# Kernel optimization log

Hardware: AMD Instinct MI355X
Metric: run time of the kernel (lower is better)

## Reference

```python
import jax, jax.numpy as jnp
import numpy as np

D_MODEL = 1024
D_FF = 4096
N_EXPERTS = 8
TOP_K = 2

def setup_inputs() -> dict:
    key = jax.random.key(0)
    ks = jax.random.split(key, 8)
    s = 1.0 / np.sqrt(D_MODEL)
    sf = 1.0 / np.sqrt(D_FF)
    return {
        "x": jax.random.normal(ks[0], (4, 1024, D_MODEL), dtype=jnp.float32),
        "W1": jax.random.uniform(ks[1], (N_EXPERTS, D_MODEL, D_FF), jnp.float32, -s, s),
        "b1": jax.random.uniform(ks[2], (N_EXPERTS, D_FF), jnp.float32, -s, s),
        "W2": jax.random.uniform(ks[3], (N_EXPERTS, D_FF, D_MODEL), jnp.float32, -sf, sf),
        "b2": jax.random.uniform(ks[4], (N_EXPERTS, D_MODEL), jnp.float32, -sf, sf),
        "Wg": jax.random.uniform(ks[5], (D_MODEL, N_EXPERTS), jnp.float32, -s, s),
        "bg": jax.random.uniform(ks[6], (N_EXPERTS,), jnp.float32, -s, s),
    }

def reference(x, W1, b1, W2, b2, Wg, bg):
    # gate: [B,S,E]
    logits = jnp.einsum('bsd,de->bse', x, Wg) + bg
    probs = jax.nn.softmax(logits, axis=-1)
    # top-k mask + renormalize (k < n_experts)
    topk_vals, topk_idx = jax.lax.top_k(probs, TOP_K)
    mask = jax.nn.one_hot(topk_idx, N_EXPERTS, dtype=probs.dtype).sum(axis=-2)
    probs = probs * mask
    denom = probs.sum(axis=-1, keepdims=True)
    denom = denom + (denom == 0).astype(probs.dtype)
    probs = probs / denom
    # dense expert compute: all experts on all tokens. h: [B,E,S,d_ff]
    h = jnp.einsum('bsd,edf->besf', x, W1) + b1[None, :, None, :]
    h = jax.nn.gelu(h, approximate=False)
    y = jnp.einsum('besf,efd->besd', h, W2) + b2[None, :, None, :]
    # weighted combine over experts: [B,S,d]
    out = jnp.einsum('bse,besd->bsd', probs, y)
    return out
```

## Files before the change

### kernel.cpp

```cpp
#include <hip/hip_runtime.h>
#include <hip/hip_bf16.h>

#define NTOK   4096
#define DMODEL 1024
#define DFF    4096
#define NEXP   8
#define TOPK   2
#define BM 128
#define BN 128
#define BK 64
#define NSLOT   (NTOK*TOPK)
#define MAXSLOT (NSLOT + NEXP*BM)
#define MAXTILE (MAXSLOT/BM)

typedef __attribute__((ext_vector_type(8))) short bf16x8;
typedef __attribute__((ext_vector_type(8))) unsigned short u16x8;
typedef __attribute__((ext_vector_type(4))) float f32x4;

__device__ __forceinline__ unsigned short f2bf(float f){
    union { float f; unsigned int u; } v; v.f = f;
    unsigned int r = (v.u + 0x7fffu + ((v.u >> 16) & 1u)) >> 16;
    return (unsigned short)r;
}

__device__ __forceinline__ void gload16(const unsigned short* g, unsigned short* l){
    __builtin_amdgcn_global_load_lds(
        (const __attribute__((address_space(1))) void*)g,
        (__attribute__((address_space(3))) void*)l,
        16, 0, 0);
}

__global__ __launch_bounds__(256) void k_transpose_convert(const float* __restrict__ src,
                                                           unsigned short* __restrict__ dst,
                                                           int R, int C)
{
    __shared__ unsigned short tile[64][72];
    src += (size_t)blockIdx.z * R * C;
    dst += (size_t)blockIdx.z * R * C;
    int r0 = blockIdx.y * 64, c0 = blockIdx.x * 64;
    int t = threadIdx.x;
    int tr = t >> 4;
    int tc = (t & 15) * 4;
    #pragma unroll
    for(int i=0;i<4;i++){
        float4 v = *(const float4*)&src[(size_t)(r0 + tr + i*16)*C + c0 + tc];
        tile[tc+0][tr + i*16] = f2bf(v.x);
        tile[tc+1][tr + i*16] = f2bf(v.y);
        tile[tc+2][tr + i*16] = f2bf(v.z);
        tile[tc+3][tr + i*16] = f2bf(v.w);
    }
    __syncthreads();
    int rr  = t >> 3;
    int cc8 = (t & 7) * 8;
    #pragma unroll
    for(int i=0;i<2;i++){
        u16x8 o = *(const u16x8*)&tile[rr + i*32][cc8];
        *(u16x8*)&dst[(size_t)(c0 + rr + i*32)*R + r0 + cc8] = o;
    }
}

__global__ __launch_bounds__(256) void k_gate(const float* __restrict__ x,
                                              const float* __restrict__ Wg,
                                              const float* __restrict__ bg,
                                              unsigned short* __restrict__ Xb,
                                              int* __restrict__ token_e,
                                              float* __restrict__ token_w,
                                              int* __restrict__ cnt)
{
    int tid = threadIdx.x;
    const float4* xs = (const float4*)x + (size_t)blockIdx.x * 1024;
    ushort4* xd = (ushort4*)Xb + (size_t)blockIdx.x * 1024;
    #pragma unroll
    for(int rep=0;rep<4;rep++){
        float4 v = xs[rep*256 + tid];
        ushort4 o; o.x=f2bf(v.x); o.y=f2bf(v.y); o.z=f2bf(v.z); o.w=f2bf(v.w);
        xd[rep*256 + tid] = o;
    }

    int wid = tid >> 6, lane = tid & 63;
    int t = blockIdx.x * 4 + wid;
    const float* xr = x + (size_t)t * DMODEL;
    float pe[NEXP];
    #pragma unroll
    for(int e=0;e<NEXP;e++) pe[e] = 0.f;
    for(int i=0;i<DMODEL/64;i++){
        int d = i*64 + lane;
        float xv = xr[d];
        const float* wr = Wg + (size_t)d * NEXP;
        #pragma unroll
        for(int e=0;e<NEXP;e++) pe[e] += xv * wr[e];
    }
    #pragma unroll
    for(int off=32; off>0; off>>=1){
        #pragma unroll
        for(int e=0;e<NEXP;e++) pe[e] += __shfl_xor(pe[e], off);
    }
    if(lane == 0){
        float lg[NEXP], mx = -1e30f;
        #pragma unroll
        for(int e=0;e<NEXP;e++){ lg[e] = pe[e] + bg[e]; mx = fmaxf(mx, lg[e]); }
        float pr[NEXP];
        #pragma unroll
        for(int e=0;e<NEXP;e++) pr[e] = expf(lg[e] - mx);
        int e0 = 0; float p0 = pr[0];
        #pragma unroll
        for(int e=1;e<NEXP;e++) if(pr[e] > p0){ p0 = pr[e]; e0 = e; }
        int e1 = -1; float p1 = -1.f;
        #pragma unroll
        for(int e=0;e<NEXP;e++) if(e != e0 && pr[e] > p1){ p1 = pr[e]; e1 = e; }
        float dn = p0 + p1;
        token_e[2*t]   = e0; token_w[2*t]   = p0/dn;
        token_e[2*t+1] = e1; token_w[2*t+1] = p1/dn;
        atomicAdd(&cnt[e0], 1); atomicAdd(&cnt[e1], 1);
    }
}

__global__ __launch_bounds__(256) void k_prefix_scatter(const int* __restrict__ cnt,
                                                        const int* __restrict__ token_e,
                                                        const float* __restrict__ token_w,
                                                        int* __restrict__ tile_e,
                                                        int* __restrict__ tile_row0,
                                                        int* __restrict__ tile_valid,
                                                        int* __restrict__ slot_token,
                                                        float* __restrict__ slot_w)
{
    __shared__ int sb[NEXP], scur[NEXP];
    int tid = threadIdx.x;
    if(tid == 0){
        int off = 0, nt = 0;
        for(int e=0;e<NEXP;e++){
            sb[e] = off; scur[e] = 0;
            int c = cnt[e];
            for(int r=0;r<c;r+=BM){
                tile_e[nt] = e; tile_row0[nt] = off + r;
                tile_valid[nt] = (c - r < BM) ? (c - r) : BM;
                nt++;
            }
            off += ((c + BM - 1)/BM)*BM;
        }
        for(int i=nt;i<MAXTILE;i++){ tile_e[i]=0; tile_row0[i]=0; tile_valid[i]=0; }
    }
    for(int s=tid; s<MAXSLOT; s+=256) slot_token[s] = 0;
    __syncthreads();
    for(int i=tid; i<NSLOT; i+=256){
        int e = token_e[i];
        int s = sb[e] + atomicAdd(&scur[e], 1);
        slot_token[s] = i >> 1;
        slot_w[s] = token_w[i];
    }
}

template<bool GATHER, bool GELU>
__global__ __launch_bounds__(256) void k_gemm(const unsigned short* __restrict__ A,
                                              const unsigned short* __restrict__ Bw,
                                              const float* __restrict__ bias,
                                              const int* __restrict__ tile_e,
                                              const int* __restrict__ tile_row0,
                                              const int* __restrict__ tile_valid,
                                              const int* __restrict__ slot_token,
                                              const float* __restrict__ slot_w,
                                              unsigned short* __restrict__ OutH,
                                              float* __restrict__ outF,
                                              int K, int N)
{
    int tid = blockIdx.x;
    int valid = tile_valid[tid];
    if(valid == 0) return;
    int e = tile_e[tid];
    int row0 = tile_row0[tid];
    int n0 = blockIdx.y * BN;
    const unsigned short* Be = Bw + (size_t)e * N * K;

    __shared__ unsigned short As[BM*BK];
    __shared__ unsigned short Bs[BN*BK];

    int t = threadIdx.x;
    int lane = t & 63;
    int wid = t >> 6;
    int wr = wid >> 1, wc = wid & 1;

    int srow = t >> 3;
    int csw  = (t & 7) ^ (srow & 7);
    const unsigned short* arow[4];
    const unsigned short* brow[4];
    #pragma unroll
    for(int i=0;i<4;i++){
        int r = i*32 + srow;
        size_t aoff;
        if(GATHER) aoff = (size_t)slot_token[row0 + r] * (size_t)K;
        else       aoff = (size_t)(row0 + r) * (size_t)K;
        arow[i] = A  + aoff + csw*8;
        brow[i] = Be + (size_t)(n0 + r)*K + csw*8;
    }
    unsigned short* alds = As + (size_t)t * 8;
    unsigned short* blds = Bs + (size_t)t * 8;

    f32x4 acc[4][4];
    #pragma unroll
    for(int m=0;m<4;m++)
        #pragma unroll
        for(int n=0;n<4;n++)
            acc[m][n] = (f32x4){0.f,0.f,0.f,0.f};

    int rl = lane & 15;
    int g  = lane >> 4;
    int rx = rl & 7;

    for(int k0=0;k0<K;k0+=BK){
        __syncthreads();
        #pragma unroll
        for(int i=0;i<4;i++){
            gload16(arow[i] + k0, alds + i*2048);
            gload16(brow[i] + k0, blds + i*2048);
        }
        __syncthreads();

        #pragma unroll
        for(int kb=0;kb<2;kb++){
            int sw = ((kb*4 + g) ^ rx) * 8;
            bf16x8 af[4], bfv[4];
            #pragma unroll
            for(int m=0;m<4;m++) af[m]  = *(const bf16x8*)&As[(wr*64 + m*16 + rl)*BK + sw];
            #pragma unroll
            for(int n=0;n<4;n++) bfv[n] = *(const bf16x8*)&Bs[(wc*64 + n*16 + rl)*BK + sw];
            #pragma unroll
            for(int m=0;m<4;m++)
                #pragma unroll
                for(int n=0;n<4;n++)
                    acc[m][n] = __builtin_amdgcn_mfma_f32_16x16x32_bf16(af[m], bfv[n], acc[m][n], 0, 0, 0);
        }
    }

    const float* be = bias + (size_t)e * N;
    #pragma unroll
    for(int m=0;m<4;m++){
        int rb = wr*64 + m*16 + ((lane>>4)<<2);
        #pragma unroll
        for(int j=0;j<4;j++){
            int r = rb + j;
            if(r >= valid) continue;
            size_t grow = (size_t)(row0 + r);
            if(GELU){
                #pragma unroll
                for(int n=0;n<4;n++){
                    int col = n0 + wc*64 + n*16 + rl;
                    float v = acc[m][n][j] + be[col];
                    v = 0.5f * v * (1.f + erff(v * 0.70710678118654752f));
                    OutH[grow * (size_t)N + col] = f2bf(v);
                }
            } else {
                float wsc = slot_w[grow];
                float* orow = outF + (size_t)slot_token[grow] * DMODEL;
                #pragma unroll
                for(int n=0;n<4;n++){
                    int col = n0 + wc*64 + n*16 + rl;
                    float v = (acc[m][n][j] + be[col]) * wsc;
                    atomicAdd(&orow[col], v);
                }
            }
        }
    }
}

extern "C" void kernel_launch(void* const* d_in, const int* in_sizes, int n_in,
                              void* d_out, int out_size, void* d_ws, size_t ws_size,
                              hipStream_t stream)
{
    const float* x  = (const float*)d_in[0];
    const float* W1 = (const float*)d_in[1];
    const float* b1 = (const float*)d_in[2];
    const float* W2 = (const float*)d_in[3];
    const float* b2 = (const float*)d_in[4];
    const float* Wg = (const float*)d_in[5];
    const float* bg = (const float*)d_in[6];
    float* out = (float*)d_out;

    char* p = (char*)d_ws;
    auto alloc = [&](size_t bytes)->char*{
        char* r = p; p += (bytes + 255) & ~(size_t)255; return r;
    };
    unsigned short* W1t = (unsigned short*)alloc((size_t)NEXP*DFF*DMODEL*2);
    unsigned short* W2t = (unsigned short*)alloc((size_t)NEXP*DMODEL*DFF*2);
    unsigned short* Xb  = (unsigned short*)alloc((size_t)NTOK*DMODEL*2);
    unsigned short* H   = (unsigned short*)alloc((size_t)MAXSLOT*DFF*2);
    int*   slot_token = (int*)alloc(MAXSLOT*4);
    float* slot_w     = (float*)alloc(MAXSLOT*4);
    int*   token_e    = (int*)alloc(NSLOT*4);
    float* token_w    = (float*)alloc(NSLOT*4);
    int*   cnt        = (int*)alloc(32);
    int*   tile_e     = (int*)alloc(MAXTILE*4);
    int*   tile_row0  = (int*)alloc(MAXTILE*4);
    int*   tile_valid = (int*)alloc(MAXTILE*4);
    (void)ws_size; (void)in_sizes; (void)n_in; (void)out_size;

    hipMemsetAsync(cnt, 0, 32, stream);
    hipMemsetAsync(out, 0, (size_t)NTOK*DMODEL*4, stream);
    k_gate<<<NTOK/4, 256, 0, stream>>>(x, Wg, bg, Xb, token_e, token_w, cnt);
    k_transpose_convert<<<dim3(DFF/64, DMODEL/64, NEXP), 256, 0, stream>>>(W1, W1t, DMODEL, DFF);
    k_transpose_convert<<<dim3(DMODEL/64, DFF/64, NEXP), 256, 0, stream>>>(W2, W2t, DFF, DMODEL);
    k_prefix_scatter<<<1, 256, 0, stream>>>(cnt, token_e, token_w,
                                            tile_e, tile_row0, tile_valid,
                                            slot_token, slot_w);
    k_gemm<true, true ><<<dim3(MAXTILE, DFF/BN),    256, 0, stream>>>(
        Xb, W1t, b1, tile_e, tile_row0, tile_valid, slot_token, slot_w, H, nullptr, DMODEL, DFF);
    k_gemm<false,false><<<dim3(MAXTILE, DMODEL/BN), 256, 0, stream>>>(
        H,  W2t, b2, tile_e, tile_row0, tile_valid, slot_token, slot_w, nullptr, out, DFF, DMODEL);
}
```

Baseline: 502.6 us.

## Double-buffer LDS tiles with async prefetch two stages ahead in grouped GEMM

Replaces the single-buffered BK=64 main loop with a double-buffered BK=32 pipeline that issues global-to-LDS loads for tile k+2 while MFMAs run on tile k. It uses explicit vmcnt/lgkmcnt waits, raw s_barrier with sched_barrier pins, and s_setprio around the MFMA block. The swizzle is reworked for the 32-wide rows. The aim is to hide global load latency behind compute, at the cost of more barriers per K and a smaller K step per iteration. The hand-placed waits must exactly match the number of outstanding loads, or the kernel reads stale data.

Measured after the change: 560.4 us. 11.5% more time.

```diff
diff --git a/kernel.cpp b/kernel.cpp
--- a/kernel.cpp
+++ b/kernel.cpp
@@ -8,7 +8,7 @@
 #define TOPK   2
 #define BM 128
 #define BN 128
-#define BK 64
+#define BK 32
 #define NSLOT   (NTOK*TOPK)
 #define MAXSLOT (NSLOT + NEXP*BM)
 #define MAXTILE (MAXSLOT/BM)
@@ -29,6 +29,12 @@
         (__attribute__((address_space(3))) void*)l,
         16, 0, 0);
 }
+
+#define WAITLGKM() asm volatile("s_waitcnt lgkmcnt(0)" ::: "memory")
+#define WAITVM4()  asm volatile("s_waitcnt vmcnt(4)" ::: "memory")
+#define WAITVM0()  asm volatile("s_waitcnt vmcnt(0)" ::: "memory")
+#define SCHEDPIN() __builtin_amdgcn_sched_barrier(0)
+#define MFMA16(a,b,c) __builtin_amdgcn_mfma_f32_16x16x32_bf16(a,b,c,0,0,0)
 
 __global__ __launch_bounds__(256) void k_transpose_convert(const float* __restrict__ src,
                                                            unsigned short* __restrict__ dst,
@@ -171,29 +177,32 @@
     int n0 = blockIdx.y * BN;
     const unsigned short* Be = Bw + (size_t)e * N * K;
 
-    __shared__ unsigned short As[BM*BK];
-    __shared__ unsigned short Bs[BN*BK];
+    __shared__ unsigned short lds[16384];
 
     int t = threadIdx.x;
     int lane = t & 63;
     int wid = t >> 6;
     int wr = wid >> 1, wc = wid & 1;
 
-    int srow = t >> 3;
-    int csw  = (t & 7) ^ (srow & 7);
-    const unsigned short* arow[4];
-    const unsigned short* brow[4];
-    #pragma unroll
-    for(int i=0;i<4;i++){
-        int r = i*32 + srow;
+    int r0s = t >> 2;
+    int csw = (t & 3) ^ ((t >> 3) & 3);
+    const unsigned short* arow[2];
+    const unsigned short* brow[2];
+    #pragma unroll
+    for(int i=0;i<2;i++){
+        int r = i*64 + r0s;
         size_t aoff;
         if(GATHER) aoff = (size_t)slot_token[row0 + r] * (size_t)K;
         else       aoff = (size_t)(row0 + r) * (size_t)K;
         arow[i] = A  + aoff + csw*8;
         brow[i] = Be + (size_t)(n0 + r)*K + csw*8;
     }
-    unsigned short* alds = As + (size_t)t * 8;
-    unsigned short* blds = Bs + (size_t)t * 8;
+
+#define STAGE(kt) { int bb = ((kt)&1)*8192; \
+    gload16(arow[0] + (kt)*32, &lds[bb        + t*8]); \
+    gload16(arow[1] + (kt)*32, &lds[bb + 2048 + t*8]); \
+    gload16(brow[0] + (kt)*32, &lds[bb + 4096 + t*8]); \
+    gload16(brow[1] + (kt)*32, &lds[bb + 6144 + t*8]); }
 
     f32x4 acc[4][4];
     #pragma unroll
@@ -204,37 +213,43 @@
 
     int rl = lane & 15;
     int g  = lane >> 4;
-    int rx = rl & 7;
-
-    for(int k0=0;k0<K;k0+=BK){
-        __syncthreads();
-        #pragma unroll
-        for(int i=0;i<4;i++){
-            gload16(arow[i] + k0, alds + i*2048);
-            gload16(brow[i] + k0, blds + i*2048);
-        }
-        __syncthreads();
-
-        #pragma unroll
-        for(int kb=0;kb<2;kb++){
-            int sw = ((kb*4 + g) ^ rx) * 8;
-            bf16x8 af[4], bfv[4];
+    int swr = (g ^ ((rl >> 1) & 3)) * 8;
+
+    STAGE(0); STAGE(1);
+    WAITVM4();
+    __builtin_amdgcn_s_barrier();
+    SCHEDPIN();
+
+    int NK = K >> 5;
+    for(int k=0;k<NK;k++){
+        int bb = (k & 1) * 8192;
+        bf16x8 af[4], bfv[4];
+        #pragma unroll
+        for(int m=0;m<4;m++) af[m]  = *(const bf16x8*)&lds[bb        + (wr*64 + m*16 + rl)*32 + swr];
+        #pragma unroll
+        for(int n=0;n<4;n++) bfv[n] = *(const bf16x8*)&lds[bb + 4096 + (wc*64 + n*16 + rl)*32 + swr];
+        WAITLGKM();
+        __builtin_amdgcn_s_barrier();
+        SCHEDPIN();
+        if(k+2 < NK) STAGE(k+2);
+        __builtin_amdgcn_s_setprio(1);
+        #pragma unroll
+        for(int m=0;m<4;m++)
             #pragma unroll
-            for(int m=0;m<4;m++) af[m]  = *(const bf16x8*)&As[(wr*64 + m*16 + rl)*BK + sw];
-            #pragma unroll
-            for(int n=0;n<4;n++) bfv[n] = *(const bf16x8*)&Bs[(wc*64 + n*16 + rl)*BK + sw];
-            #pragma unroll
-            for(int m=0;m<4;m++)
-                #pragma unroll
-                for(int n=0;n<4;n++)
-                    acc[m][n] = __builtin_amdgcn_mfma_f32_16x16x32_bf16(af[m], bfv[n], acc[m][n], 0, 0, 0);
-        }
-    }
+            for(int n=0;n<4;n++)
+                acc[m][n] = MFMA16(af[m], bfv[n], acc[m][n]);
+        __builtin_amdgcn_s_setprio(0);
+        if(k+2 < NK)      { WAITVM4(); }
+        else if(k+1 < NK) { WAITVM0(); }
+        __builtin_amdgcn_s_barrier();
+        SCHEDPIN();
+    }
+#undef STAGE
 
     const float* be = bias + (size_t)e * N;
     #pragma unroll
     for(int m=0;m<4;m++){
-        int rb = wr*64 + m*16 + ((lane>>4)<<2);
+        int rb = wr*64 + m*16 + g*4;
         #pragma unroll
         for(int j=0;j<4;j++){
             int r = rb + j;
```

## Double-buffer LDS in MoE GEMM, remap tile order, merge weight transposes

Applied to the files above, without the earlier changes.

The grouped GEMM now double-buffers its LDS tiles: the next K-slice is issued with global_load_lds before the MFMAs on the current slice, with one barrier per iteration. It also adds explicit waitcnt, sched_barrier and setprio hints. Block indices are permuted so that consecutive blocks cover tiles spread across experts, launch bounds ask for two blocks per CU, and the W1 and W2 transpose-convert kernels are merged into one launch. The aim is to hide global load latency behind MFMA work and cut one launch, at the cost of doubling LDS use to 64KB per block, which may limit occupancy.

Result: slower. 535.6 us (+6.6%).

```diff
diff --git a/kernel.cpp b/kernel.cpp
--- a/kernel.cpp
+++ b/kernel.cpp
@@ -30,14 +30,30 @@
         16, 0, 0);
 }
 
-__global__ __launch_bounds__(256) void k_transpose_convert(const float* __restrict__ src,
-                                                           unsigned short* __restrict__ dst,
-                                                           int R, int C)
+#define WAITLGKM() asm volatile("s_waitcnt lgkmcnt(0)" ::: "memory")
+#define WAITVM0()  asm volatile("s_waitcnt vmcnt(0)" ::: "memory")
+#define SCHEDPIN() __builtin_amdgcn_sched_barrier(0)
+#define MFMA16(a,b,c) __builtin_amdgcn_mfma_f32_16x16x32_bf16(a,b,c,0,0,0)
+
+__global__ __launch_bounds__(256) void k_transpose_convert2(const float* __restrict__ W1,
+                                                            const float* __restrict__ W2,
+                                                            unsigned short* __restrict__ W1t,
+                                                            unsigned short* __restrict__ W2t)
 {
     __shared__ unsigned short tile[64][72];
-    src += (size_t)blockIdx.z * R * C;
-    dst += (size_t)blockIdx.z * R * C;
-    int r0 = blockIdx.y * 64, c0 = blockIdx.x * 64;
+    int z = blockIdx.z;
+    const float* src; unsigned short* dst; int R, C, r0, c0;
+    if(z < 8){
+        src = W1  + (size_t)z * DMODEL * DFF;
+        dst = W1t + (size_t)z * DMODEL * DFF;
+        R = DMODEL; C = DFF;
+        r0 = blockIdx.y * 64; c0 = blockIdx.x * 64;
+    } else {
+        src = W2  + (size_t)(z-8) * DFF * DMODEL;
+        dst = W2t + (size_t)(z-8) * DFF * DMODEL;
+        R = DFF; C = DMODEL;
+        r0 = blockIdx.x * 64; c0 = blockIdx.y * 64;
+    }
     int t = threadIdx.x;
     int tr = t >> 4;
     int tc = (t & 15) * 4;
@@ -151,19 +167,20 @@
 }
 
 template<bool GATHER, bool GELU>
-__global__ __launch_bounds__(256) void k_gemm(const unsigned short* __restrict__ A,
-                                              const unsigned short* __restrict__ Bw,
-                                              const float* __restrict__ bias,
-                                              const int* __restrict__ tile_e,
-                                              const int* __restrict__ tile_row0,
-                                              const int* __restrict__ tile_valid,
-                                              const int* __restrict__ slot_token,
-                                              const float* __restrict__ slot_w,
-                                              unsigned short* __restrict__ OutH,
-                                              float* __restrict__ outF,
-                                              int K, int N)
-{
-    int tid = blockIdx.x;
+__global__ __launch_bounds__(256, 2) void k_gemm(const unsigned short* __restrict__ A,
+                                                 const unsigned short* __restrict__ Bw,
+                                                 const float* __restrict__ bias,
+                                                 const int* __restrict__ tile_e,
+                                                 const int* __restrict__ tile_row0,
+                                                 const int* __restrict__ tile_valid,
+                                                 const int* __restrict__ slot_token,
+                                                 const float* __restrict__ slot_w,
+                                                 unsigned short* __restrict__ OutH,
+                                                 float* __restrict__ outF,
+                                                 int K, int N)
+{
+    int xb = blockIdx.x;
+    int tid = (xb & 7) * (MAXTILE/8) + (xb >> 3);
     int valid = tile_valid[tid];
     if(valid == 0) return;
     int e = tile_e[tid];
@@ -171,8 +188,7 @@
     int n0 = blockIdx.y * BN;
     const unsigned short* Be = Bw + (size_t)e * N * K;
 
-    __shared__ unsigned short As[BM*BK];
-    __shared__ unsigned short Bs[BN*BK];
+    __shared__ unsigned short lds[32768];
 
     int t = threadIdx.x;
     int lane = t & 63;
@@ -192,8 +208,16 @@
         arow[i] = A  + aoff + csw*8;
         brow[i] = Be + (size_t)(n0 + r)*K + csw*8;
     }
-    unsigned short* alds = As + (size_t)t * 8;
-    unsigned short* blds = Bs + (size_t)t * 8;
+
+#define STAGE(kt) { int bb = ((kt)&1)*16384; \
+    gload16(arow[0] + (kt)*64, &lds[bb        + (0*256+t)*8]); \
+    gload16(arow[1] + (kt)*64, &lds[bb        + (1*256+t)*8]); \
+    gload16(arow[2] + (kt)*64, &lds[bb        + (2*256+t)*8]); \
+    gload16(arow[3] + (kt)*64, &lds[bb        + (3*256+t)*8]); \
+    gload16(brow[0] + (kt)*64, &lds[bb + 8192 + (0*256+t)*8]); \
+    gload16(brow[1] + (kt)*64, &lds[bb + 8192 + (1*256+t)*8]); \
+    gload16(brow[2] + (kt)*64, &lds[bb + 8192 + (2*256+t)*8]); \
+    gload16(brow[3] + (kt)*64, &lds[bb + 8192 + (3*256+t)*8]); }
 
     f32x4 acc[4][4];
     #pragma unroll
@@ -206,35 +230,45 @@
     int g  = lane >> 4;
     int rx = rl & 7;
 
-    for(int k0=0;k0<K;k0+=BK){
-        __syncthreads();
-        #pragma unroll
-        for(int i=0;i<4;i++){
-            gload16(arow[i] + k0, alds + i*2048);
-            gload16(brow[i] + k0, blds + i*2048);
-        }
-        __syncthreads();
-
+    STAGE(0);
+    WAITVM0();
+    __builtin_amdgcn_s_barrier();
+    SCHEDPIN();
+
+    int NK = K >> 6;
+    for(int k=0;k<NK;k++){
+        int bb = (k & 1) * 16384;
+        if(k+1 < NK) STAGE(k+1);
+        bf16x8 af[2][4], bfv[2][4];
         #pragma unroll
         for(int kb=0;kb<2;kb++){
             int sw = ((kb*4 + g) ^ rx) * 8;
-            bf16x8 af[4], bfv[4];
             #pragma unroll
-            for(int m=0;m<4;m++) af[m]  = *(const bf16x8*)&As[(wr*64 + m*16 + rl)*BK + sw];
+            for(int m=0;m<4;m++) af[kb][m]  = *(const bf16x8*)&lds[bb        + (wr*64 + m*16 + rl)*64 + sw];
             #pragma unroll
-            for(int n=0;n<4;n++) bfv[n] = *(const bf16x8*)&Bs[(wc*64 + n*16 + rl)*BK + sw];
+            for(int n=0;n<4;n++) bfv[kb][n] = *(const bf16x8*)&lds[bb + 8192 + (wc*64 + n*16 + rl)*64 + sw];
+        }
+        WAITLGKM();
+        SCHEDPIN();
+        __builtin_amdgcn_s_setprio(1);
+        #pragma unroll
+        for(int kb=0;kb<2;kb++)
             #pragma unroll
             for(int m=0;m<4;m++)
                 #pragma unroll
                 for(int n=0;n<4;n++)
-                    acc[m][n] = __builtin_amdgcn_mfma_f32_16x16x32_bf16(af[m], bfv[n], acc[m][n], 0, 0, 0);
-        }
-    }
+                    acc[m][n] = MFMA16(af[kb][m], bfv[kb][n], acc[m][n]);
+        __builtin_amdgcn_s_setprio(0);
+        WAITVM0();
+        __builtin_amdgcn_s_barrier();
+        SCHEDPIN();
+    }
+#undef STAGE
 
     const float* be = bias + (size_t)e * N;
     #pragma unroll
     for(int m=0;m<4;m++){
-        int rb = wr*64 + m*16 + ((lane>>4)<<2);
+        int rb = wr*64 + m*16 + g*4;
         #pragma unroll
         for(int j=0;j<4;j++){
             int r = rb + j;
@@ -296,8 +330,7 @@
     hipMemsetAsync(cnt, 0, 32, stream);
     hipMemsetAsync(out, 0, (size_t)NTOK*DMODEL*4, stream);
     k_gate<<<NTOK/4, 256, 0, stream>>>(x, Wg, bg, Xb, token_e, token_w, cnt);
-    k_transpose_convert<<<dim3(DFF/64, DMODEL/64, NEXP), 256, 0, stream>>>(W1, W1t, DMODEL, DFF);
-    k_transpose_convert<<<dim3(DMODEL/64, DFF/64, NEXP), 256, 0, stream>>>(W2, W2t, DFF, DMODEL);
+    k_transpose_convert2<<<dim3(DFF/64, DMODEL/64, 16), 256, 0, stream>>>(W1, W2, W1t, W2t);
     k_prefix_scatter<<<1, 256, 0, stream>>>(cnt, token_e, token_w,
                                             tile_e, tile_row0, tile_valid,
                                             slot_token, slot_w);
```

## Merge weight transposes, remap GEMM tile order, and cap registers for occupancy

Applied to the files above, without the earlier changes.

Both weight transpose-convert passes now run as one launch over a 16-deep z grid, with the W2 half swapping block coordinates so one grid shape covers both. The GEMM now interleaves its block index so consecutive blocks come from different expert tile ranges, and its launch bounds request three waves per SIMD to allow more resident blocks. The aims are to save a launch, spread tile work and weight traffic evenly, and hide latency better. The occupancy cap could force register spills in the 4x4 MFMA accumulator kernel.

Result: faster. 481.1 us (-4.3%).

```diff
diff --git a/kernel.cpp b/kernel.cpp
--- a/kernel.cpp
+++ b/kernel.cpp
@@ -30,14 +30,25 @@
         16, 0, 0);
 }
 
-__global__ __launch_bounds__(256) void k_transpose_convert(const float* __restrict__ src,
-                                                           unsigned short* __restrict__ dst,
-                                                           int R, int C)
+__global__ __launch_bounds__(256) void k_transpose_convert2(const float* __restrict__ W1,
+                                                            const float* __restrict__ W2,
+                                                            unsigned short* __restrict__ W1t,
+                                                            unsigned short* __restrict__ W2t)
 {
     __shared__ unsigned short tile[64][72];
-    src += (size_t)blockIdx.z * R * C;
-    dst += (size_t)blockIdx.z * R * C;
-    int r0 = blockIdx.y * 64, c0 = blockIdx.x * 64;
+    int z = blockIdx.z;
+    const float* src; unsigned short* dst; int R, C, r0, c0;
+    if(z < 8){
+        src = W1  + (size_t)z * DMODEL * DFF;
+        dst = W1t + (size_t)z * DMODEL * DFF;
+        R = DMODEL; C = DFF;
+        r0 = blockIdx.y * 64; c0 = blockIdx.x * 64;
+    } else {
+        src = W2  + (size_t)(z-8) * DFF * DMODEL;
+        dst = W2t + (size_t)(z-8) * DFF * DMODEL;
+        R = DFF; C = DMODEL;
+        r0 = blockIdx.x * 64; c0 = blockIdx.y * 64;
+    }
     int t = threadIdx.x;
     int tr = t >> 4;
     int tc = (t & 15) * 4;
@@ -151,19 +162,20 @@
 }
 
 template<bool GATHER, bool GELU>
-__global__ __launch_bounds__(256) void k_gemm(const unsigned short* __restrict__ A,
-                                              const unsigned short* __restrict__ Bw,
-                                              const float* __restrict__ bias,
-                                              const int* __restrict__ tile_e,
-                                              const int* __restrict__ tile_row0,
-                                              const int* __restrict__ tile_valid,
-                                              const int* __restrict__ slot_token,
-                                              const float* __restrict__ slot_w,
-                                              unsigned short* __restrict__ OutH,
-                                              float* __restrict__ outF,
-                                              int K, int N)
-{
-    int tid = blockIdx.x;
+__global__ __launch_bounds__(256, 3) void k_gemm(const unsigned short* __restrict__ A,
+                                                 const unsigned short* __restrict__ Bw,
+                                                 const float* __restrict__ bias,
+                                                 const int* __restrict__ tile_e,
+                                                 const int* __restrict__ tile_row0,
+                                                 const int* __restrict__ tile_valid,
+                                                 const int* __restrict__ slot_token,
+                                                 const float* __restrict__ slot_w,
+                                                 unsigned short* __restrict__ OutH,
+                                                 float* __restrict__ outF,
+                                                 int K, int N)
+{
+    int xb = blockIdx.x;
+    int tid = (xb & 7) * (MAXTILE/8) + (xb >> 3);
     int valid = tile_valid[tid];
     if(valid == 0) return;
     int e = tile_e[tid];
@@ -234,7 +246,7 @@
     const float* be = bias + (size_t)e * N;
     #pragma unroll
     for(int m=0;m<4;m++){
-        int rb = wr*64 + m*16 + ((lane>>4)<<2);
+        int rb = wr*64 + m*16 + g*4;
         #pragma unroll
         for(int j=0;j<4;j++){
             int r = rb + j;
@@ -296,8 +308,7 @@
     hipMemsetAsync(cnt, 0, 32, stream);
     hipMemsetAsync(out, 0, (size_t)NTOK*DMODEL*4, stream);
     k_gate<<<NTOK/4, 256, 0, stream>>>(x, Wg, bg, Xb, token_e, token_w, cnt);
-    k_transpose_convert<<<dim3(DFF/64, DMODEL/64, NEXP), 256, 0, stream>>>(W1, W1t, DMODEL, DFF);
-    k_transpose_convert<<<dim3(DMODEL/64, DFF/64, NEXP), 256, 0, stream>>>(W2, W2t, DFF, DMODEL);
+    k_transpose_convert2<<<dim3(DFF/64, DMODEL/64, 16), 256, 0, stream>>>(W1, W2, W1t, W2t);
     k_prefix_scatter<<<1, 256, 0, stream>>>(cnt, token_e, token_w,
                                             tile_e, tile_row0, tile_valid,
                                             slot_token, slot_w);
```
